# Performance work log

Hardware: AMD Instinct MI355X
Metric: run time of the kernel (lower is better)

## Reference

```python
import jax, jax.numpy as jnp
import numpy as np

N_NODES = 131072      # total nodes across all graphs
IN_CHANNELS = 256     # node attribute dim after continuous WL embedding
NUM_PROJ = 256        # num_projections
NUM_QUANT = 256       # num_quantiles
NUM_GRAPHS = 256      # batch of graphs (equal-sized segments of 512 nodes)
P_NORM = 2            # p-sliced Wasserstein


def setup_inputs() -> dict:
    key = jax.random.key(0)
    k1, k2 = jax.random.split(key)
    x = jax.random.normal(k1, (N_NODES, IN_CHANNELS), dtype=jnp.float32)
    # fixed random projections, column-normalized (resample_projections)
    projections = jax.random.normal(k2, (IN_CHANNELS, NUM_PROJ), dtype=jnp.float32)
    projections = projections / jnp.sqrt(jnp.sum(projections ** 2, axis=0, keepdims=True))
    # cum_weights buffer: linspace(0, 1, num_quantiles)
    cum_weights = jnp.linspace(0.0, 1.0, NUM_QUANT, dtype=jnp.float32)
    # equal-sized graph segments (sorted segment ids), jit-friendly
    batch = (jnp.arange(N_NODES, dtype=jnp.int32) // (N_NODES // NUM_GRAPHS))
    return {
        "x": x,
        "projections": projections,
        "cum_weights": cum_weights,
        "batch": batch,
        "num_graphs": NUM_GRAPHS,
    }


def reference(x, projections, cum_weights, batch, num_graphs):
    # x: [N, C], projections: [C, P], cum_weights: [Q]
    n_nodes = x.shape[0]
    num_p = projections.shape[1]
    num_q = cum_weights.shape[0]
    nodes_per_graph = n_nodes // num_graphs

    xp = jnp.matmul(x, projections)                       # [N, P]
    xg = xp.reshape(num_graphs, nodes_per_graph, num_p)   # [B, n, P]
    xs = jnp.sort(xg, axis=1)                             # segmented sort per graph
    # torch.quantile(..., interpolation='lower'): index = floor(q * (n-1))
    idx = jnp.floor(cum_weights * (nodes_per_graph - 1)).astype(jnp.int32)  # [Q]
    quant = xs[:, idx, :]                                 # [B, Q, P]
    scale = (num_q * num_p) ** (1.0 / P_NORM)
    return quant.reshape(num_graphs, num_q * num_p) / scale
```

## Files before the change

### kernel.cpp

```cpp
#include <hip/hip_runtime.h>
#include <hip/hip_bf16.h>
#include <hip/hip_fp16.h>

typedef unsigned short u16;
typedef unsigned int u32;
typedef __bf16 bf16x8 __attribute__((ext_vector_type(8)));
typedef float f32x4 __attribute__((ext_vector_type(4)));
typedef u16 u16x8 __attribute__((ext_vector_type(8)));


__device__ __forceinline__ u16 f2bf(float f) {
  union { float f; u32 u; } v; v.f = f;
  u32 r = (v.u + 0x7FFFu + ((v.u >> 16) & 1u)) >> 16;
  return (u16)r;
}

__device__ __forceinline__ u32 cvtpk(float a, float b) {
  u32 r; asm("v_cvt_pk_bf16_f32 %0, %1, %2" : "=v"(r) : "v"(a), "v"(b));
  return r;
}

__device__ __forceinline__ void gl16(const void* g, void* l) {
  __builtin_amdgcn_global_load_lds((const __attribute__((address_space(1))) unsigned int*)g,
                                   (__attribute__((address_space(3))) unsigned int*)l,
                                   16, 0, 0);
}

__device__ __forceinline__ u32 pkmin(u32 a, u32 b) {
  u32 r; asm("v_pk_min_f16 %0, %1, %2" : "=v"(r) : "v"(a), "v"(b)); return r;
}
__device__ __forceinline__ u32 pkmax(u32 a, u32 b) {
  u32 r; asm("v_pk_max_f16 %0, %1, %2" : "=v"(r) : "v"(a), "v"(b)); return r;
}

template <int CTRL> __device__ __forceinline__ u32 xdpp(u32 x) {
  return (u32)__builtin_amdgcn_mov_dpp((int)x, CTRL, 0xF, 0xF, true);
}
template <int IMM> __device__ __forceinline__ u32 xswz(u32 x) {
  return (u32)__builtin_amdgcn_ds_swizzle((int)x, IMM);
}
#define EX_X1(x)  xdpp<0xB1>(x)
#define EX_X2(x)  xdpp<0x4E>(x)
#define EX_F3(x)  xdpp<0x1B>(x)
#define EX_F7(x)  xdpp<0x141>(x)
#define EX_F15(x) xdpp<0x140>(x)
#define EX_X8(x)  xdpp<0x128>(x)
#define EX_X4(x)  xswz<0x101F>(x)
#define EX_X16(x) xswz<0x401F>(x)
#define EX_F31(x) xswz<0x7C1F>(x)
#define EX_F63(x) ((u32)__shfl_xor((int)(x), 63, 64))

__global__ __launch_bounds__(256) void transpose_proj(const float* __restrict__ proj,
                                                      u16* __restrict__ projT) {
  const int k = blockIdx.x;
  const int p = threadIdx.x;
  projT[(size_t)p * 256 + k] = f2bf(proj[(size_t)k * 256 + p]);
}

__global__ __launch_bounds__(256) void gemm_xt(const float* __restrict__ x,
                                               const u16* __restrict__ projT,
                                               __half* __restrict__ xp16) {
  __shared__ u16 As[128 * 32];
  __shared__ float Bs[128 * 32];

  const int tid = threadIdx.x;
  const int bid = blockIdx.x;
  const int slot = bid & 7;
  const int j = bid >> 3;
  const int p0 = (j & 1) * 128;
  const int n0 = (slot + (j >> 1) * 8) * 128;
  const int lane = tid & 63;
  const int w = tid >> 6;
  const int wp = (w >> 1) * 64;
  const int wn = (w & 1) * 64;
  const int quad = lane >> 4;
  const int m16 = lane & 15;

  const u16* asrc0 = projT + (size_t)(p0 + (2 * w) * 16 + (lane >> 2)) * 256 + (lane & 3) * 8;
  const u16* asrc1 = asrc0 + 16 * 256;
  u16* adst0 = &As[(2 * w) * 512];
  u16* adst1 = &As[(2 * w + 1) * 512];
  const float* bsrc0 = x + (size_t)(n0 + (4 * w) * 8 + (lane >> 3)) * 256 + (lane & 7) * 4;
  const float* bsrc1 = bsrc0 + 8 * 256;
  const float* bsrc2 = bsrc0 + 16 * 256;
  const float* bsrc3 = bsrc0 + 24 * 256;
  float* bdst0 = &Bs[(4 * w) * 256];
  float* bdst1 = &Bs[(4 * w + 1) * 256];
  float* bdst2 = &Bs[(4 * w + 2) * 256];
  float* bdst3 = &Bs[(4 * w + 3) * 256];

  f32x4 acc[4][4];
#pragma unroll
  for (int i = 0; i < 4; ++i)
#pragma unroll
    for (int jj = 0; jj < 4; ++jj) acc[i][jj] = (f32x4){0.f, 0.f, 0.f, 0.f};

  for (int k0 = 0; k0 < 256; k0 += 32) {
    gl16(bsrc0 + k0, bdst0);
    gl16(bsrc1 + k0, bdst1);
    gl16(bsrc2 + k0, bdst2);
    gl16(bsrc3 + k0, bdst3);
    gl16(asrc0 + k0, adst0);
    gl16(asrc1 + k0, adst1);
    __syncthreads();

    bf16x8 af[4], bfv[4];
#pragma unroll
    for (int mi = 0; mi < 4; ++mi)
      af[mi] = *(const bf16x8*)&As[(wp + mi * 16 + m16) * 32 + quad * 8];
#pragma unroll
    for (int ni = 0; ni < 4; ++ni) {
      const float* bp = &Bs[(wn + ni * 16 + m16) * 32 + quad * 8];
      float4 f0 = *(const float4*)bp;
      float4 f1 = *(const float4*)(bp + 4);
      u32 pk[4] = { cvtpk(f0.x, f0.y), cvtpk(f0.z, f0.w),
                    cvtpk(f1.x, f1.y), cvtpk(f1.z, f1.w) };
      bfv[ni] = *(const bf16x8*)pk;
    }
#pragma unroll
    for (int mi = 0; mi < 4; ++mi)
#pragma unroll
      for (int ni = 0; ni < 4; ++ni)
        acc[mi][ni] = __builtin_amdgcn_mfma_f32_16x16x32_bf16(af[mi], bfv[ni], acc[mi][ni], 0, 0, 0);
    __syncthreads();
  }

#pragma unroll
  for (int mi = 0; mi < 4; ++mi) {
#pragma unroll
    for (int r = 0; r < 4; ++r) {
      const int p = p0 + wp + mi * 16 + quad * 4 + r;
      __half* dst = xp16 + (size_t)p * 131072 + (n0 + wn + m16);
#pragma unroll
      for (int ni = 0; ni < 4; ++ni) dst[ni * 16] = __float2half(acc[mi][ni][r]);
    }
  }
}

__global__ __launch_bounds__(1024) void sort_sel(const __half* __restrict__ xp16,
                                                 const float* __restrict__ cw,
                                                 float* __restrict__ out) {
  __shared__ u32 sbuf[16][520];
  const int tid = threadIdx.x;
  const int lane = tid & 63;
  const int w = tid >> 6;
  const int bid = blockIdx.x;
  const int g = bid >> 3;
  const int pt = bid & 7;
  const int p_lo = pt * 32 + w;
  const int p_hi = p_lo + 16;

  const u16* slo = (const u16*)(xp16 + (size_t)p_lo * 131072 + (size_t)g * 512) + lane * 8;
  const u16* shi = (const u16*)(xp16 + (size_t)p_hi * 131072 + (size_t)g * 512) + lane * 8;
  u16x8 lo = *(const u16x8*)slo;
  u16x8 hi = *(const u16x8*)shi;
  u32 v[8];
#pragma unroll
  for (int r = 0; r < 8; ++r) v[r] = (u32)lo[r] | ((u32)hi[r] << 16);

#define CE(i, j) { u32 mn_ = pkmin(v[i], v[j]); u32 mx_ = pkmax(v[i], v[j]); v[i] = mn_; v[j] = mx_; }
#define INTRA3 \
  CE(0,4) CE(1,5) CE(2,6) CE(3,7) \
  CE(0,2) CE(1,3) CE(4,6) CE(5,7) \
  CE(0,1) CE(2,3) CE(4,5) CE(6,7)

#define FLIPP(EX, lowbit) { \
    const bool low_ = (lane & (lowbit)) == 0; \
    u32 t_[8]; \
    _Pragma("unroll") for (int r = 0; r < 8; ++r) t_[r] = EX(v[7 - r]); \
    _Pragma("unroll") for (int r = 0; r < 8; ++r) { \
      u32 mn_ = pkmin(v[r], t_[r]); u32 mx_ = pkmax(v[r], t_[r]); \
      v[r] = low_ ? mn_ : mx_; } }

#define XCROSSP(EX, lm) { \
    const bool low_ = (lane & (lm)) == 0; \
    _Pragma("unroll") for (int r = 0; r < 8; ++r) { \
      u32 t_ = EX(v[r]); \
      u32 mn_ = pkmin(v[r], t_); u32 mx_ = pkmax(v[r], t_); \
      v[r] = low_ ? mn_ : mx_; } }

  CE(0,1) CE(2,3) CE(4,5) CE(6,7)
  CE(0,3) CE(1,2) CE(4,7) CE(5,6)
  CE(0,1) CE(2,3) CE(4,5) CE(6,7)
  CE(0,7) CE(1,6) CE(2,5) CE(3,4)
  CE(0,2) CE(1,3) CE(4,6) CE(5,7)
  CE(0,1) CE(2,3) CE(4,5) CE(6,7)
  FLIPP(EX_X1, 1)  INTRA3
  FLIPP(EX_F3, 2)  XCROSSP(EX_X1, 1)  INTRA3
  FLIPP(EX_F7, 4)  XCROSSP(EX_X2, 2) XCROSSP(EX_X1, 1)  INTRA3
  FLIPP(EX_F15, 8) XCROSSP(EX_X4, 4) XCROSSP(EX_X2, 2) XCROSSP(EX_X1, 1)  INTRA3
  FLIPP(EX_F31, 16) XCROSSP(EX_X8, 8) XCROSSP(EX_X4, 4) XCROSSP(EX_X2, 2) XCROSSP(EX_X1, 1)  INTRA3
  FLIPP(EX_F63, 32) XCROSSP(EX_X16, 16) XCROSSP(EX_X8, 8) XCROSSP(EX_X4, 4) XCROSSP(EX_X2, 2) XCROSSP(EX_X1, 1)  INTRA3

#undef CE
#undef INTRA3
#undef FLIPP
#undef XCROSSP

  *(uint4*)&sbuf[w][lane * 8]     = (uint4){v[0], v[1], v[2], v[3]};
  *(uint4*)&sbuf[w][lane * 8 + 4] = (uint4){v[4], v[5], v[6], v[7]};
  __syncthreads();

  const float scale = 1.0f / 256.0f;
#pragma unroll
  for (int it = 0; it < 8; ++it) {
    const int linear = it * 1024 + tid;
    const int q = linear >> 5;
    const int pl = linear & 31;
    const int iq = (int)floorf(cw[q] * 511.0f);
    const u32 val = sbuf[pl & 15][iq];
    const u16 h = (pl & 16) ? (u16)(val >> 16) : (u16)(val & 0xFFFF);
    __half_raw hr; hr.x = h;
    out[(size_t)g * 65536 + (size_t)q * 256 + pt * 32 + pl] = __half2float(__half(hr)) * scale;
  }
}

extern "C" void kernel_launch(void* const* d_in, const int* in_sizes, int n_in,
                              void* d_out, int out_size, void* d_ws, size_t ws_size,
                              hipStream_t stream) {
  const float* x    = (const float*)d_in[0];
  const float* proj = (const float*)d_in[1];
  const float* cw   = (const float*)d_in[2];
  float* out = (float*)d_out;

  __half* xp16 = (__half*)d_ws;
  u16* projT = (u16*)((char*)d_ws + (size_t)64 * 1024 * 1024);

  transpose_proj<<<256, 256, 0, stream>>>(proj, projT);
  gemm_xt<<<2048, 256, 0, stream>>>(x, projT, xp16);
  sort_sel<<<2048, 1024, 0, stream>>>(xp16, cw, out);
}
```

Measured before the change: 286.9 us.

## Fuse projection GEMM with per-graph bitonic sort and quantile gather

Replaces the separate GEMM and sort kernels with one kernel per graph. Each block loads its graph's 512 node rows into bf16 MFMA operands held in registers, computes 64 projections at a time into LDS as fp16, sorts them with the existing packed bitonic network and writes the selected quantiles. This removes the 64MB fp16 intermediate round trip through global memory. The cost is only 256 blocks of 1024 threads with about 97KB of LDS each, which lowers occupancy and parallelism and serialises four projection quarters per block.

```diff
diff --git a/kernel.cpp b/kernel.cpp
--- a/kernel.cpp
+++ b/kernel.cpp
@@ -1,12 +1,10 @@
 #include <hip/hip_runtime.h>
-#include <hip/hip_bf16.h>
 #include <hip/hip_fp16.h>
 
 typedef unsigned short u16;
 typedef unsigned int u32;
 typedef __bf16 bf16x8 __attribute__((ext_vector_type(8)));
 typedef float f32x4 __attribute__((ext_vector_type(4)));
-typedef u16 u16x8 __attribute__((ext_vector_type(8)));
 
 
 __device__ __forceinline__ u16 f2bf(float f) {
@@ -20,10 +18,14 @@
   return r;
 }
 
-__device__ __forceinline__ void gl16(const void* g, void* l) {
-  __builtin_amdgcn_global_load_lds((const __attribute__((address_space(1))) unsigned int*)g,
-                                   (__attribute__((address_space(3))) unsigned int*)l,
-                                   16, 0, 0);
+__device__ __forceinline__ u32 pkh(float a, float b) {
+  return (u32)__half_as_ushort(__float2half(a)) |
+         ((u32)__half_as_ushort(__float2half(b)) << 16);
+}
+
+__device__ __forceinline__ u32 vperm(u32 s0, u32 s1, u32 sel) {
+  u32 r; asm("v_perm_b32 %0, %1, %2, %3" : "=v"(r) : "v"(s0), "v"(s1), "s"(sel));
+  return r;
 }
 
 __device__ __forceinline__ u32 pkmin(u32 a, u32 b) {
@@ -57,106 +59,80 @@
   projT[(size_t)p * 256 + k] = f2bf(proj[(size_t)k * 256 + p]);
 }
 
-__global__ __launch_bounds__(256) void gemm_xt(const float* __restrict__ x,
-                                               const u16* __restrict__ projT,
-                                               __half* __restrict__ xp16) {
-  __shared__ u16 As[128 * 32];
-  __shared__ float Bs[128 * 32];
-
-  const int tid = threadIdx.x;
-  const int bid = blockIdx.x;
-  const int slot = bid & 7;
-  const int j = bid >> 3;
-  const int p0 = (j & 1) * 128;
-  const int n0 = (slot + (j >> 1) * 8) * 128;
-  const int lane = tid & 63;
-  const int w = tid >> 6;
-  const int wp = (w >> 1) * 64;
-  const int wn = (w & 1) * 64;
-  const int quad = lane >> 4;
-  const int m16 = lane & 15;
-
-  const u16* asrc0 = projT + (size_t)(p0 + (2 * w) * 16 + (lane >> 2)) * 256 + (lane & 3) * 8;
-  const u16* asrc1 = asrc0 + 16 * 256;
-  u16* adst0 = &As[(2 * w) * 512];
-  u16* adst1 = &As[(2 * w + 1) * 512];
-  const float* bsrc0 = x + (size_t)(n0 + (4 * w) * 8 + (lane >> 3)) * 256 + (lane & 7) * 4;
-  const float* bsrc1 = bsrc0 + 8 * 256;
-  const float* bsrc2 = bsrc0 + 16 * 256;
-  const float* bsrc3 = bsrc0 + 24 * 256;
-  float* bdst0 = &Bs[(4 * w) * 256];
-  float* bdst1 = &Bs[(4 * w + 1) * 256];
-  float* bdst2 = &Bs[(4 * w + 2) * 256];
-  float* bdst3 = &Bs[(4 * w + 3) * 256];
-
-  f32x4 acc[4][4];
-#pragma unroll
-  for (int i = 0; i < 4; ++i)
-#pragma unroll
-    for (int jj = 0; jj < 4; ++jj) acc[i][jj] = (f32x4){0.f, 0.f, 0.f, 0.f};
-
-  for (int k0 = 0; k0 < 256; k0 += 32) {
-    gl16(bsrc0 + k0, bdst0);
-    gl16(bsrc1 + k0, bdst1);
-    gl16(bsrc2 + k0, bdst2);
-    gl16(bsrc3 + k0, bdst3);
-    gl16(asrc0 + k0, adst0);
-    gl16(asrc1 + k0, adst1);
-    __syncthreads();
-
-    bf16x8 af[4], bfv[4];
-#pragma unroll
-    for (int mi = 0; mi < 4; ++mi)
-      af[mi] = *(const bf16x8*)&As[(wp + mi * 16 + m16) * 32 + quad * 8];
-#pragma unroll
-    for (int ni = 0; ni < 4; ++ni) {
-      const float* bp = &Bs[(wn + ni * 16 + m16) * 32 + quad * 8];
-      float4 f0 = *(const float4*)bp;
-      float4 f1 = *(const float4*)(bp + 4);
-      u32 pk[4] = { cvtpk(f0.x, f0.y), cvtpk(f0.z, f0.w),
-                    cvtpk(f1.x, f1.y), cvtpk(f1.z, f1.w) };
-      bfv[ni] = *(const bf16x8*)pk;
-    }
-#pragma unroll
-    for (int mi = 0; mi < 4; ++mi)
-#pragma unroll
-      for (int ni = 0; ni < 4; ++ni)
-        acc[mi][ni] = __builtin_amdgcn_mfma_f32_16x16x32_bf16(af[mi], bfv[ni], acc[mi][ni], 0, 0, 0);
-    __syncthreads();
-  }
-
-#pragma unroll
-  for (int mi = 0; mi < 4; ++mi) {
-#pragma unroll
-    for (int r = 0; r < 4; ++r) {
-      const int p = p0 + wp + mi * 16 + quad * 4 + r;
-      __half* dst = xp16 + (size_t)p * 131072 + (n0 + wn + m16);
-#pragma unroll
-      for (int ni = 0; ni < 4; ++ni) dst[ni * 16] = __float2half(acc[mi][ni][r]);
-    }
-  }
-}
-
-__global__ __launch_bounds__(1024) void sort_sel(const __half* __restrict__ xp16,
-                                                 const float* __restrict__ cw,
-                                                 float* __restrict__ out) {
-  __shared__ u32 sbuf[16][520];
+__global__ __launch_bounds__(1024) void fused_swe(const float* __restrict__ x,
+                                                  const u16* __restrict__ projT,
+                                                  const float* __restrict__ cw,
+                                                  float* __restrict__ out) {
+  extern __shared__ __attribute__((aligned(16))) char lds[];
+  u32* res = (u32*)(lds + 32768);
+
   const int tid = threadIdx.x;
   const int lane = tid & 63;
   const int w = tid >> 6;
-  const int bid = blockIdx.x;
-  const int g = bid >> 3;
-  const int pt = bid & 7;
-  const int p_lo = pt * 32 + w;
-  const int p_hi = p_lo + 16;
-
-  const u16* slo = (const u16*)(xp16 + (size_t)p_lo * 131072 + (size_t)g * 512) + lane * 8;
-  const u16* shi = (const u16*)(xp16 + (size_t)p_hi * 131072 + (size_t)g * 512) + lane * 8;
-  u16x8 lo = *(const u16x8*)slo;
-  u16x8 hi = *(const u16x8*)shi;
-  u32 v[8];
-#pragma unroll
-  for (int r = 0; r < 8; ++r) v[r] = (u32)lo[r] | ((u32)hi[r] << 16);
+  const int g = blockIdx.x;
+  const int quad = lane >> 4;
+  const int m16 = lane & 15;
+
+  bf16x8 a[2][8];
+#pragma unroll
+  for (int t = 0; t < 2; ++t) {
+    const float* ap = x + (size_t)(g * 512 + w * 32 + t * 16 + m16) * 256 + quad * 8;
+#pragma unroll
+    for (int ks = 0; ks < 8; ++ks) {
+      float4 f0 = *(const float4*)(ap + ks * 32);
+      float4 f1 = *(const float4*)(ap + ks * 32 + 4);
+      u32 pk4[4] = { cvtpk(f0.x, f0.y), cvtpk(f0.z, f0.w),
+                     cvtpk(f1.x, f1.y), cvtpk(f1.z, f1.w) };
+      a[t][ks] = *(const bf16x8*)pk4;
+    }
+  }
+
+  for (int qtr = 0; qtr < 4; ++qtr) {
+    {
+      const int row = tid >> 4;
+      const int seg0 = tid & 15;
+#pragma unroll
+      for (int si = 0; si < 2; ++si) {
+        const int seg = seg0 + si * 16;
+        uint4 d = *(const uint4*)(projT + (size_t)(qtr * 64 + row) * 256 + seg * 8);
+        *(uint4*)(lds + row * 512 + ((seg ^ (row & 7)) * 16)) = d;
+      }
+    }
+    __syncthreads();
+
+#pragma unroll
+    for (int nt = 0; nt < 4; ++nt) {
+      const int prow = nt * 16 + m16;
+      const int rx = (prow & 7) << 4;
+      const char* pb = lds + prow * 512;
+      f32x4 acc0 = {0.f, 0.f, 0.f, 0.f};
+      f32x4 acc1 = {0.f, 0.f, 0.f, 0.f};
+#pragma unroll
+      for (int ks = 0; ks < 8; ++ks) {
+        bf16x8 bfrag = *(const bf16x8*)(pb + (((ks * 64) | (quad * 16)) ^ rx));
+        acc0 = __builtin_amdgcn_mfma_f32_16x16x32_bf16(a[0][ks], bfrag, acc0, 0, 0, 0);
+        acc1 = __builtin_amdgcn_mfma_f32_16x16x32_bf16(a[1][ks], bfrag, acc1, 0, 0, 0);
+      }
+      const int wb = prow * 260 + w * 16 + quad * 2;
+      res[wb]     = pkh(acc0[0], acc0[1]);
+      res[wb + 1] = pkh(acc0[2], acc0[3]);
+      res[wb + 8] = pkh(acc1[0], acc1[1]);
+      res[wb + 9] = pkh(acc1[2], acc1[3]);
+    }
+    __syncthreads();
+
+#pragma unroll
+    for (int s = 0; s < 2; ++s) {
+      const int d = w * 2 + s;
+      u32* ra = res + d * 260;
+      u32* rb = res + (d + 32) * 260;
+      uint4 a4 = *(const uint4*)(ra + lane * 4);
+      uint4 b4 = *(const uint4*)(rb + lane * 4);
+      u32 v[8];
+      v[0] = vperm(b4.x, a4.x, 0x05040100u); v[1] = vperm(b4.x, a4.x, 0x07060302u);
+      v[2] = vperm(b4.y, a4.y, 0x05040100u); v[3] = vperm(b4.y, a4.y, 0x07060302u);
+      v[4] = vperm(b4.z, a4.z, 0x05040100u); v[5] = vperm(b4.z, a4.z, 0x07060302u);
+      v[6] = vperm(b4.w, a4.w, 0x05040100u); v[7] = vperm(b4.w, a4.w, 0x07060302u);
 
 #define CE(i, j) { u32 mn_ = pkmin(v[i], v[j]); u32 mx_ = pkmax(v[i], v[j]); v[i] = mn_; v[j] = mx_; }
 #define INTRA3 \
@@ -179,39 +155,43 @@
       u32 mn_ = pkmin(v[r], t_); u32 mx_ = pkmax(v[r], t_); \
       v[r] = low_ ? mn_ : mx_; } }
 
-  CE(0,1) CE(2,3) CE(4,5) CE(6,7)
-  CE(0,3) CE(1,2) CE(4,7) CE(5,6)
-  CE(0,1) CE(2,3) CE(4,5) CE(6,7)
-  CE(0,7) CE(1,6) CE(2,5) CE(3,4)
-  CE(0,2) CE(1,3) CE(4,6) CE(5,7)
-  CE(0,1) CE(2,3) CE(4,5) CE(6,7)
-  FLIPP(EX_X1, 1)  INTRA3
-  FLIPP(EX_F3, 2)  XCROSSP(EX_X1, 1)  INTRA3
-  FLIPP(EX_F7, 4)  XCROSSP(EX_X2, 2) XCROSSP(EX_X1, 1)  INTRA3
-  FLIPP(EX_F15, 8) XCROSSP(EX_X4, 4) XCROSSP(EX_X2, 2) XCROSSP(EX_X1, 1)  INTRA3
-  FLIPP(EX_F31, 16) XCROSSP(EX_X8, 8) XCROSSP(EX_X4, 4) XCROSSP(EX_X2, 2) XCROSSP(EX_X1, 1)  INTRA3
-  FLIPP(EX_F63, 32) XCROSSP(EX_X16, 16) XCROSSP(EX_X8, 8) XCROSSP(EX_X4, 4) XCROSSP(EX_X2, 2) XCROSSP(EX_X1, 1)  INTRA3
+      CE(0,1) CE(2,3) CE(4,5) CE(6,7)
+      CE(0,3) CE(1,2) CE(4,7) CE(5,6)
+      CE(0,1) CE(2,3) CE(4,5) CE(6,7)
+      CE(0,7) CE(1,6) CE(2,5) CE(3,4)
+      CE(0,2) CE(1,3) CE(4,6) CE(5,7)
+      CE(0,1) CE(2,3) CE(4,5) CE(6,7)
+      FLIPP(EX_X1, 1)  INTRA3
+      FLIPP(EX_F3, 2)  XCROSSP(EX_X1, 1)  INTRA3
+      FLIPP(EX_F7, 4)  XCROSSP(EX_X2, 2) XCROSSP(EX_X1, 1)  INTRA3
+      FLIPP(EX_F15, 8) XCROSSP(EX_X4, 4) XCROSSP(EX_X2, 2) XCROSSP(EX_X1, 1)  INTRA3
+      FLIPP(EX_F31, 16) XCROSSP(EX_X8, 8) XCROSSP(EX_X4, 4) XCROSSP(EX_X2, 2) XCROSSP(EX_X1, 1)  INTRA3
+      FLIPP(EX_F63, 32) XCROSSP(EX_X16, 16) XCROSSP(EX_X8, 8) XCROSSP(EX_X4, 4) XCROSSP(EX_X2, 2) XCROSSP(EX_X1, 1)  INTRA3
 
 #undef CE
 #undef INTRA3
 #undef FLIPP
 #undef XCROSSP
 
-  *(uint4*)&sbuf[w][lane * 8]     = (uint4){v[0], v[1], v[2], v[3]};
-  *(uint4*)&sbuf[w][lane * 8 + 4] = (uint4){v[4], v[5], v[6], v[7]};
-  __syncthreads();
-
-  const float scale = 1.0f / 256.0f;
-#pragma unroll
-  for (int it = 0; it < 8; ++it) {
-    const int linear = it * 1024 + tid;
-    const int q = linear >> 5;
-    const int pl = linear & 31;
-    const int iq = (int)floorf(cw[q] * 511.0f);
-    const u32 val = sbuf[pl & 15][iq];
-    const u16 h = (pl & 16) ? (u16)(val >> 16) : (u16)(val & 0xFFFF);
-    __half_raw hr; hr.x = h;
-    out[(size_t)g * 65536 + (size_t)q * 256 + pt * 32 + pl] = __half2float(__half(hr)) * scale;
+      u32* pp = (lane < 32) ? (ra + lane * 8) : (rb + lane * 8 - 256);
+      *(uint4*)pp       = (uint4){v[0], v[1], v[2], v[3]};
+      *(uint4*)(pp + 4) = (uint4){v[4], v[5], v[6], v[7]};
+    }
+    __syncthreads();
+
+#pragma unroll
+    for (int it = 0; it < 16; ++it) {
+      const int linear = it * 1024 + tid;
+      const int q = linear >> 6;
+      const int pc = linear & 63;
+      const int iq = (int)floorf(cw[q] * 511.0f);
+      const int dd = pc & 31;
+      const u32 val = res[dd * 260 + ((iq >= 256) ? (iq + 8064) : iq)];
+      const u16 h = (pc & 32) ? (u16)(val >> 16) : (u16)(val & 0xFFFF);
+      __half_raw hr; hr.x = h;
+      out[(size_t)g * 65536 + (size_t)q * 256 + qtr * 64 + pc] =
+          __half2float(__half(hr)) * 0.00390625f;
+    }
   }
 }
 
@@ -223,10 +203,8 @@
   const float* cw   = (const float*)d_in[2];
   float* out = (float*)d_out;
 
-  __half* xp16 = (__half*)d_ws;
-  u16* projT = (u16*)((char*)d_ws + (size_t)64 * 1024 * 1024);
+  u16* projT = (u16*)d_ws;
 
   transpose_proj<<<256, 256, 0, stream>>>(proj, projT);
-  gemm_xt<<<2048, 256, 0, stream>>>(x, projT, xp16);
-  sort_sel<<<2048, 1024, 0, stream>>>(xp16, cw, out);
-}
+  fused_swe<<<256, 1024, 99328, stream>>>(x, projT, cw, out);
+}
```

Result: no change. 284.3 us (-0.9%).
